# Kernel optimization log

Measured on AMD Instinct MI355X. Metric: run time of the kernel, lower is better.

The kernel has to match this reference:

```python
import jax, jax.numpy as jnp
import numpy as np

EMBED_DIM = 1024
NUM_HEADS = 16
HEAD_DIM = EMBED_DIM // NUM_HEADS


def setup_inputs() -> dict:
    key = jax.random.key(0)
    ks = jax.random.split(key, 9)
    d = EMBED_DIM
    # flax Dense default: lecun_normal kernel init ~ scale 1/sqrt(fan_in), zero bias
    s = 1.0 / np.sqrt(d)
    return {
        "x": jax.random.normal(ks[0], (4, 2048, d), dtype=jnp.float32),
        "Wq": jax.random.normal(ks[1], (d, d), dtype=jnp.float32) * s,
        "bq": jnp.zeros((d,), dtype=jnp.float32),
        "Wk": jax.random.normal(ks[2], (d, d), dtype=jnp.float32) * s,
        "bk": jnp.zeros((d,), dtype=jnp.float32),
        "Wv": jax.random.normal(ks[3], (d, d), dtype=jnp.float32) * s,
        "bv": jnp.zeros((d,), dtype=jnp.float32),
        "Wo": jax.random.normal(ks[4], (d, d), dtype=jnp.float32) * s,
        "bo": jnp.zeros((d,), dtype=jnp.float32),
    }


def reference(x, Wq, bq, Wk, bk, Wv, bv, Wo, bo):
    B, S, D = x.shape
    H, Hd = NUM_HEADS, HEAD_DIM

    def split_heads(t):
        # [B,S,D] -> [B,H,S,Hd]
        return t.reshape(B, S, H, Hd).swapaxes(1, 2)

    q = split_heads(x @ Wq + bq)
    k = split_heads(x @ Wk + bk)
    v = split_heads(x @ Wv + bv)

    # [B,H,S,S] attention logits, scaled by sqrt(head_dim)
    attn_logits = jnp.einsum("bhqd,bhkd->bhqk", q, k) / jnp.sqrt(
        jnp.asarray(Hd, dtype=x.dtype)
    )
    attn = jax.nn.softmax(attn_logits, axis=-1)
    # dropout rate = 0.0 / deterministic=True -> identity

    values = jnp.einsum("bhqk,bhkd->bhqd", attn, v)  # [B,H,S,Hd]
    values = values.swapaxes(1, 2).reshape(B, S, D)  # [B,S,D]
    return values @ Wo + bo
```

## Files before the change

kernel.cpp:

```cpp
#include <hip/hip_runtime.h>
#include <hip/hip_bf16.h>
#include <cstdint>

typedef __attribute__((ext_vector_type(8))) short short8;
typedef __attribute__((ext_vector_type(4))) float f32x4;
typedef __attribute__((ext_vector_type(4))) int int4v;
typedef unsigned short ushort_t;

#define D_MODEL 1024
#define SEQ     2048
#define NBATCH  4
#define NHEADS  16
#define HDIM    64

__device__ __forceinline__ unsigned short f2bf(float f) {
  unsigned int u = __float_as_uint(f);
  u = u + 0x7fffu + ((u >> 16) & 1u);
  return (unsigned short)(u >> 16);
}

__device__ __forceinline__ float exp2_fast(float x) {
  return __builtin_amdgcn_exp2f(x);
}

__device__ __forceinline__ unsigned int cvtpk(float lo, float hi) {
  unsigned int r;
  asm("v_cvt_pk_bf16_f32 %0, %1, %2" : "=v"(r) : "v"(lo), "v"(hi));
  return r;
}

typedef __attribute__((address_space(1))) const void gv_t;
typedef __attribute__((address_space(3))) void lv_t;
__device__ __forceinline__ void gload16(const void* g, void* l) {
  __builtin_amdgcn_global_load_lds((gv_t*)g, (lv_t*)l, 16, 0, 0);
}

__global__ __launch_bounds__(256) void cvt_x_kernel(const float* __restrict__ x,
                                                    ushort_t* __restrict__ xb) {
  int i = blockIdx.x * 256 + threadIdx.x;
  float4 v = reinterpret_cast<const float4*>(x)[i];
  ushort4 o;
  o.x = f2bf(v.x); o.y = f2bf(v.y); o.z = f2bf(v.z); o.w = f2bf(v.w);
  reinterpret_cast<ushort4*>(xb)[i] = o;
}

__global__ __launch_bounds__(256) void cvt_w_kernel(const float* __restrict__ Wq,
                                                    const float* __restrict__ Wk,
                                                    const float* __restrict__ Wv,
                                                    const float* __restrict__ Wo,
                                                    ushort_t* __restrict__ WTqkv,
                                                    ushort_t* __restrict__ WTo) {
  __shared__ float tile[64][65];
  const int z = blockIdx.z;
  const float* W = (z == 0) ? Wq : (z == 1) ? Wk : (z == 2) ? Wv : Wo;
  ushort_t* out = (z < 3) ? (WTqkv + (size_t)z * D_MODEL * D_MODEL) : WTo;
  const int k0 = blockIdx.x * 64, n0 = blockIdx.y * 64;
  const int tx = threadIdx.x & 63, ty = threadIdx.x >> 6;
#pragma unroll
  for (int i = 0; i < 16; ++i) {
    int r = ty + i * 4;
    tile[r][tx] = W[(size_t)(k0 + r) * D_MODEL + n0 + tx];
  }
  __syncthreads();
#pragma unroll
  for (int i = 0; i < 16; ++i) {
    int r = ty + i * 4;
    out[(size_t)(n0 + r) * D_MODEL + k0 + tx] = f2bf(tile[tx][r]);
  }
}

#define BM 128
#define BN 128
#define BK 32
#define QSCALE 0.18033688011112042f

__global__ __launch_bounds__(256) void gemm_qkv_kernel(
    const ushort_t* __restrict__ A, const ushort_t* __restrict__ BT,
    const float* __restrict__ bq, const float* __restrict__ bk,
    const float* __restrict__ bv,
    ushort_t* __restrict__ Qb, ushort_t* __restrict__ Kb,
    ushort_t* __restrict__ Vb) {
  __shared__ __align__(16) ushort_t As[BM * BK];
  __shared__ __align__(16) ushort_t Bs[BN * BK];
  const int t = threadIdx.x;
  const int l = t & 63;
  const int w = t >> 6;
  const int m0 = blockIdx.x * BM;
  const int n0 = blockIdx.y * BN;
  const int wm = (w & 1) * 64, wn = (w >> 1) * 64;
  const int lr = l & 15, lg = l >> 4;

  f32x4 acc[4][4] = {};

  for (int k0 = 0; k0 < D_MODEL; k0 += BK) {
#pragma unroll
    for (int i = 0; i < 2; ++i) {
      int chunk = t + i * 256;
      int row = chunk >> 2;
      int c8 = (chunk & 3) * 8;
      gload16(A  + (size_t)(m0 + row) * D_MODEL + k0 + c8, As + chunk * 8);
      gload16(BT + (size_t)(n0 + row) * D_MODEL + k0 + c8, Bs + chunk * 8);
    }
    __syncthreads();
    short8 af[4], bfr[4];
#pragma unroll
    for (int m = 0; m < 4; ++m)
      af[m] = *reinterpret_cast<const short8*>(As + (wm + m * 16 + lr) * BK + lg * 8);
#pragma unroll
    for (int n = 0; n < 4; ++n)
      bfr[n] = *reinterpret_cast<const short8*>(Bs + (wn + n * 16 + lr) * BK + lg * 8);
#pragma unroll
    for (int m = 0; m < 4; ++m)
#pragma unroll
      for (int n = 0; n < 4; ++n)
        acc[m][n] = __builtin_amdgcn_mfma_f32_16x16x32_bf16(af[m], bfr[n], acc[m][n], 0, 0, 0);
    __syncthreads();
  }

#pragma unroll
  for (int m = 0; m < 4; ++m)
#pragma unroll
    for (int n = 0; n < 4; ++n) {
      int colg = n0 + wn + n * 16 + lr;
      int which = colg >> 10;
      int nc = colg & 1023;
      int h = nc >> 6, hd = nc & 63;
      float bias = (which == 0) ? bq[nc] : (which == 1) ? bk[nc] : bv[nc];
#pragma unroll
      for (int r = 0; r < 4; ++r) {
        int rowg = m0 + wm + m * 16 + lg * 4 + r;
        int b = rowg >> 11, s = rowg & 2047;
        int bh = b * NHEADS + h;
        float vall = acc[m][n][r] + bias;
        if (which == 0) {
          Qb[((size_t)bh * SEQ + s) * HDIM + hd] = f2bf(vall * QSCALE);
        } else if (which == 1) {
          Kb[((size_t)bh * SEQ + s) * HDIM + hd] = f2bf(vall);
        } else {
          Vb[((size_t)bh * HDIM + hd) * SEQ + s] = f2bf(vall);
        }
      }
    }
}

#define KVB 64

__device__ __forceinline__ int kmap(int p) {
  return ((p >> 5) << 5) + (((p >> 2) & 3) << 3) + (((p >> 4) & 1) << 2) + (p & 3);
}

__global__ __launch_bounds__(256) void attn_kernel(const ushort_t* __restrict__ Qb,
                                                   const ushort_t* __restrict__ Kb,
                                                   const ushort_t* __restrict__ Vb,
                                                   ushort_t* __restrict__ Ob) {
  __shared__ __align__(16) ushort_t Kt[2][KVB * HDIM];
  __shared__ __align__(16) ushort_t Vt[2][HDIM * KVB];
  const int t = threadIdx.x, l = t & 63, w = t >> 6;
  const int lr = l & 15, lg = l >> 4;
  const int bh = blockIdx.x;
  const int q0 = blockIdx.y * 64;
  const int b = bh >> 4, h = bh & 15;

  const ushort_t* Qp = Qb + ((size_t)bh * SEQ + q0 + w * 16) * HDIM;
  const ushort_t* Kp = Kb + (size_t)bh * SEQ * HDIM;
  const ushort_t* Vp = Vb + (size_t)bh * HDIM * SEQ;

  const int c0 = t, c1 = t + 256;
  const int r0 = c0 >> 3, col0 = ((c0 & 7) ^ (r0 & 7)) * 8;
  const int r1 = c1 >> 3, col1 = ((c1 & 7) ^ (r1 & 7)) * 8;
  const int kr0 = kmap(r0), kr1 = kmap(r1);

  short8 aq[2];
#pragma unroll
  for (int kk = 0; kk < 2; ++kk)
    aq[kk] = *reinterpret_cast<const short8*>(Qp + lr * HDIM + kk * 32 + lg * 8);

  f32x4 o[4] = {};
  float lsum = 0.f;

  gload16(Kp + (size_t)kr0 * HDIM + col0, &Kt[0][c0 * 8]);
  gload16(Kp + (size_t)kr1 * HDIM + col1, &Kt[0][c1 * 8]);
  gload16(Vp + (size_t)r0 * SEQ + col0, &Vt[0][c0 * 8]);
  gload16(Vp + (size_t)r1 * SEQ + col1, &Vt[0][c1 * 8]);
  __syncthreads();

  int cur = 0;
  for (int kv0 = 0; kv0 < SEQ; kv0 += KVB) {
    if (kv0 + KVB < SEQ) {
      int kvn = kv0 + KVB;
      gload16(Kp + (size_t)(kvn + kr0) * HDIM + col0, &Kt[cur ^ 1][c0 * 8]);
      gload16(Kp + (size_t)(kvn + kr1) * HDIM + col1, &Kt[cur ^ 1][c1 * 8]);
      gload16(Vp + (size_t)r0 * SEQ + kvn + col0, &Vt[cur ^ 1][c0 * 8]);
      gload16(Vp + (size_t)r1 * SEQ + kvn + col1, &Vt[cur ^ 1][c1 * 8]);
    }
    const ushort_t* Kc = Kt[cur];
    const ushort_t* Vc = Vt[cur];
    f32x4 s[4];
#pragma unroll
    for (int n = 0; n < 4; ++n) s[n] = (f32x4){-16.f, -16.f, -16.f, -16.f};
#pragma unroll
    for (int n = 0; n < 4; ++n)
#pragma unroll
      for (int kk = 0; kk < 2; ++kk) {
        short8 ak = *reinterpret_cast<const short8*>(
            Kc + (n * 16 + lr) * HDIM + ((kk * 32 + lg * 8) ^ ((lr & 7) << 3)));
        s[n] = __builtin_amdgcn_mfma_f32_16x16x32_bf16(ak, aq[kk], s[n], 0, 0, 0);
      }
    float ps = 0.f;
#pragma unroll
    for (int n = 0; n < 4; ++n)
#pragma unroll
      for (int r = 0; r < 4; ++r) {
        float p = exp2_fast(s[n][r]);
        s[n][r] = p;
        ps += p;
      }
    ps += __shfl_xor(ps, 16, 64);
    ps += __shfl_xor(ps, 32, 64);
    lsum += ps;
    int4v w0, w1;
    w0[0] = cvtpk(s[0][0], s[0][1]); w0[1] = cvtpk(s[0][2], s[0][3]);
    w0[2] = cvtpk(s[1][0], s[1][1]); w0[3] = cvtpk(s[1][2], s[1][3]);
    w1[0] = cvtpk(s[2][0], s[2][1]); w1[1] = cvtpk(s[2][2], s[2][3]);
    w1[2] = cvtpk(s[3][0], s[3][1]); w1[3] = cvtpk(s[3][2], s[3][3]);
    short8 pb0 = *reinterpret_cast<short8*>(&w0);
    short8 pb1 = *reinterpret_cast<short8*>(&w1);
#pragma unroll
    for (int nd = 0; nd < 4; ++nd) {
      short8 av0 = *reinterpret_cast<const short8*>(
          Vc + (nd * 16 + lr) * KVB + ((lg * 8) ^ ((lr & 7) << 3)));
      o[nd] = __builtin_amdgcn_mfma_f32_16x16x32_bf16(av0, pb0, o[nd], 0, 0, 0);
      short8 av1 = *reinterpret_cast<const short8*>(
          Vc + (nd * 16 + lr) * KVB + ((32 + lg * 8) ^ ((lr & 7) << 3)));
      o[nd] = __builtin_amdgcn_mfma_f32_16x16x32_bf16(av1, pb1, o[nd], 0, 0, 0);
    }
    __syncthreads();
    cur ^= 1;
  }

  float inv = 1.f / lsum;
  size_t orow = ((size_t)b * SEQ + q0 + w * 16 + lr) * D_MODEL + h * HDIM;
#pragma unroll
  for (int nd = 0; nd < 4; ++nd) {
    ushort4 ov;
    ov.x = f2bf(o[nd][0] * inv);
    ov.y = f2bf(o[nd][1] * inv);
    ov.z = f2bf(o[nd][2] * inv);
    ov.w = f2bf(o[nd][3] * inv);
    *reinterpret_cast<ushort4*>(&(((ushort_t*)Ob)[orow + nd * 16 + lg * 4])) = ov;
  }
}

__global__ __launch_bounds__(256) void gemm_out_kernel(const ushort_t* __restrict__ A,
                                                       const ushort_t* __restrict__ BT,
                                                       const float* __restrict__ bo,
                                                       float* __restrict__ out) {
  __shared__ __align__(16) ushort_t As[BM * BK];
  __shared__ __align__(16) ushort_t Bs[BN * BK];
  const int t = threadIdx.x;
  const int l = t & 63;
  const int w = t >> 6;
  const int m0 = blockIdx.x * BM;
  const int n0 = blockIdx.y * BN;
  const int wm = (w & 1) * 64, wn = (w >> 1) * 64;
  const int lr = l & 15, lg = l >> 4;

  f32x4 acc[4][4] = {};

  for (int k0 = 0; k0 < D_MODEL; k0 += BK) {
#pragma unroll
    for (int i = 0; i < 2; ++i) {
      int chunk = t + i * 256;
      int row = chunk >> 2;
      int c8 = (chunk & 3) * 8;
      gload16(A  + (size_t)(m0 + row) * D_MODEL + k0 + c8, As + chunk * 8);
      gload16(BT + (size_t)(n0 + row) * D_MODEL + k0 + c8, Bs + chunk * 8);
    }
    __syncthreads();
    short8 af[4], bfr[4];
#pragma unroll
    for (int m = 0; m < 4; ++m)
      af[m] = *reinterpret_cast<const short8*>(As + (wm + m * 16 + lr) * BK + lg * 8);
#pragma unroll
    for (int n = 0; n < 4; ++n)
      bfr[n] = *reinterpret_cast<const short8*>(Bs + (wn + n * 16 + lr) * BK + lg * 8);
#pragma unroll
    for (int m = 0; m < 4; ++m)
#pragma unroll
      for (int n = 0; n < 4; ++n)
        acc[m][n] = __builtin_amdgcn_mfma_f32_16x16x32_bf16(af[m], bfr[n], acc[m][n], 0, 0, 0);
    __syncthreads();
  }

#pragma unroll
  for (int m = 0; m < 4; ++m)
#pragma unroll
    for (int n = 0; n < 4; ++n) {
      int colg = n0 + wn + n * 16 + lr;
      float bias = bo[colg];
#pragma unroll
      for (int r = 0; r < 4; ++r) {
        int rowg = m0 + wm + m * 16 + lg * 4 + r;
        out[(size_t)rowg * D_MODEL + colg] = acc[m][n][r] + bias;
      }
    }
}

extern "C" void kernel_launch(void* const* d_in, const int* in_sizes, int n_in,
                              void* d_out, int out_size, void* d_ws, size_t ws_size,
                              hipStream_t stream) {
  (void)in_sizes; (void)n_in; (void)out_size; (void)ws_size;
  const float* x  = (const float*)d_in[0];
  const float* Wq = (const float*)d_in[1];
  const float* bq = (const float*)d_in[2];
  const float* Wk = (const float*)d_in[3];
  const float* bk = (const float*)d_in[4];
  const float* Wv = (const float*)d_in[5];
  const float* bv = (const float*)d_in[6];
  const float* Wo = (const float*)d_in[7];
  const float* bo = (const float*)d_in[8];
  float* out = (float*)d_out;

  ushort_t* ws    = (ushort_t*)d_ws;
  ushort_t* WTqkv = ws;
  ushort_t* WTo   = WTqkv + 3145728;
  ushort_t* Qb    = WTo + 1048576;
  ushort_t* Kb    = Qb + 8388608;
  ushort_t* Vb    = Kb + 8388608;
  ushort_t* Ob    = Vb + 8388608;
  ushort_t* xb    = Ob;

  cvt_x_kernel<<<8192, 256, 0, stream>>>(x, xb);
  cvt_w_kernel<<<dim3(16, 16, 4), 256, 0, stream>>>(Wq, Wk, Wv, Wo, WTqkv, WTo);
  gemm_qkv_kernel<<<dim3(64, 24), 256, 0, stream>>>(xb, WTqkv, bq, bk, bv, Qb, Kb, Vb);
  attn_kernel<<<dim3(64, 32), 256, 0, stream>>>(Qb, Kb, Vb, Ob);
  gemm_out_kernel<<<dim3(64, 8), 256, 0, stream>>>(Ob, WTo, bo, out);
}
```

Baseline: 300.1 us.

## Double-buffer GEMM LDS tiles and unroll attention loop with deferred row-sum reduction

The QKV and output projection GEMMs now use two LDS buffers, so the next K tile is prefetched while the current one is consumed, with one barrier per tile instead of two. The attention loop is manually unrolled by two with static buffer indices, which removes the dynamic cur pointer. The per-tile cross-lane shuffle reduction of the softmax row sum moves to after the loop. The goal is to overlap global loads with MFMA work and to cut barrier and shuffle overhead, at the cost of doubled LDS use in the GEMMs, which may lower occupancy.

```diff
diff --git a/kernel.cpp b/kernel.cpp
--- a/kernel.cpp
+++ b/kernel.cpp
@@ -74,14 +74,42 @@
 #define BK 32
 #define QSCALE 0.18033688011112042f
 
+#define GEMM_STAGE(BUF, K0)                                                     \
+  {                                                                             \
+    _Pragma("unroll")                                                           \
+    for (int i = 0; i < 2; ++i) {                                               \
+      int chunk = t + i * 256;                                                  \
+      int row = chunk >> 2;                                                     \
+      int c8 = (chunk & 3) * 8;                                                 \
+      gload16(A  + (size_t)(m0 + row) * D_MODEL + (K0) + c8, As[BUF] + chunk * 8); \
+      gload16(BT + (size_t)(n0 + row) * D_MODEL + (K0) + c8, Bs[BUF] + chunk * 8); \
+    }                                                                           \
+  }
+
+#define GEMM_COMPUTE(BUF)                                                       \
+  {                                                                             \
+    short8 af[4], bfr[4];                                                       \
+    _Pragma("unroll")                                                           \
+    for (int m = 0; m < 4; ++m)                                                 \
+      af[m] = *reinterpret_cast<const short8*>(As[BUF] + (wm + m * 16 + lr) * BK + lg * 8); \
+    _Pragma("unroll")                                                           \
+    for (int n = 0; n < 4; ++n)                                                 \
+      bfr[n] = *reinterpret_cast<const short8*>(Bs[BUF] + (wn + n * 16 + lr) * BK + lg * 8); \
+    _Pragma("unroll")                                                           \
+    for (int m = 0; m < 4; ++m)                                                 \
+      _Pragma("unroll")                                                         \
+      for (int n = 0; n < 4; ++n)                                               \
+        acc[m][n] = __builtin_amdgcn_mfma_f32_16x16x32_bf16(af[m], bfr[n], acc[m][n], 0, 0, 0); \
+  }
+
 __global__ __launch_bounds__(256) void gemm_qkv_kernel(
     const ushort_t* __restrict__ A, const ushort_t* __restrict__ BT,
     const float* __restrict__ bq, const float* __restrict__ bk,
     const float* __restrict__ bv,
     ushort_t* __restrict__ Qb, ushort_t* __restrict__ Kb,
     ushort_t* __restrict__ Vb) {
-  __shared__ __align__(16) ushort_t As[BM * BK];
-  __shared__ __align__(16) ushort_t Bs[BN * BK];
+  __shared__ __align__(16) ushort_t As[2][BM * BK];
+  __shared__ __align__(16) ushort_t Bs[2][BN * BK];
   const int t = threadIdx.x;
   const int l = t & 63;
   const int w = t >> 6;
@@ -92,28 +120,14 @@
 
   f32x4 acc[4][4] = {};
 
-  for (int k0 = 0; k0 < D_MODEL; k0 += BK) {
-#pragma unroll
-    for (int i = 0; i < 2; ++i) {
-      int chunk = t + i * 256;
-      int row = chunk >> 2;
-      int c8 = (chunk & 3) * 8;
-      gload16(A  + (size_t)(m0 + row) * D_MODEL + k0 + c8, As + chunk * 8);
-      gload16(BT + (size_t)(n0 + row) * D_MODEL + k0 + c8, Bs + chunk * 8);
-    }
-    __syncthreads();
-    short8 af[4], bfr[4];
-#pragma unroll
-    for (int m = 0; m < 4; ++m)
-      af[m] = *reinterpret_cast<const short8*>(As + (wm + m * 16 + lr) * BK + lg * 8);
-#pragma unroll
-    for (int n = 0; n < 4; ++n)
-      bfr[n] = *reinterpret_cast<const short8*>(Bs + (wn + n * 16 + lr) * BK + lg * 8);
-#pragma unroll
-    for (int m = 0; m < 4; ++m)
-#pragma unroll
-      for (int n = 0; n < 4; ++n)
-        acc[m][n] = __builtin_amdgcn_mfma_f32_16x16x32_bf16(af[m], bfr[n], acc[m][n], 0, 0, 0);
+  GEMM_STAGE(0, 0);
+  __syncthreads();
+  for (int k0 = 0; k0 < D_MODEL; k0 += 2 * BK) {
+    if (k0 + BK < D_MODEL) GEMM_STAGE(1, k0 + BK);
+    GEMM_COMPUTE(0);
+    __syncthreads();
+    if (k0 + 2 * BK < D_MODEL) GEMM_STAGE(0, k0 + 2 * BK);
+    GEMM_COMPUTE(1);
     __syncthreads();
   }
 
@@ -149,6 +163,53 @@
   return ((p >> 5) << 5) + (((p >> 2) & 3) << 3) + (((p >> 4) & 1) << 2) + (p & 3);
 }
 
+#define ATTN_STAGE(BUF, KVN)                                                    \
+  {                                                                             \
+    gload16(Kp + (size_t)((KVN) + kr0) * HDIM + col0, &Kt[BUF][c0 * 8]);        \
+    gload16(Kp + (size_t)((KVN) + kr1) * HDIM + col1, &Kt[BUF][c1 * 8]);        \
+    gload16(Vp + (size_t)r0 * SEQ + (KVN) + col0, &Vt[BUF][c0 * 8]);            \
+    gload16(Vp + (size_t)r1 * SEQ + (KVN) + col1, &Vt[BUF][c1 * 8]);            \
+  }
+
+#define ATTN_COMPUTE(BUF)                                                       \
+  {                                                                             \
+    f32x4 s[4];                                                                 \
+    _Pragma("unroll")                                                           \
+    for (int n = 0; n < 4; ++n) s[n] = (f32x4){-16.f, -16.f, -16.f, -16.f};     \
+    _Pragma("unroll")                                                           \
+    for (int n = 0; n < 4; ++n)                                                 \
+      _Pragma("unroll")                                                         \
+      for (int kk = 0; kk < 2; ++kk) {                                          \
+        short8 ak = *reinterpret_cast<const short8*>(                           \
+            &Kt[BUF][(n * 16 + lr) * HDIM + ((kk * 32 + lg * 8) ^ ((lr & 7) << 3))]); \
+        s[n] = __builtin_amdgcn_mfma_f32_16x16x32_bf16(ak, aq[kk], s[n], 0, 0, 0); \
+      }                                                                         \
+    _Pragma("unroll")                                                           \
+    for (int n = 0; n < 4; ++n)                                                 \
+      _Pragma("unroll")                                                         \
+      for (int r = 0; r < 4; ++r) {                                             \
+        float p = exp2_fast(s[n][r]);                                           \
+        s[n][r] = p;                                                            \
+        lsum += p;                                                              \
+      }                                                                         \
+    int4v w0, w1;                                                               \
+    w0[0] = cvtpk(s[0][0], s[0][1]); w0[1] = cvtpk(s[0][2], s[0][3]);           \
+    w0[2] = cvtpk(s[1][0], s[1][1]); w0[3] = cvtpk(s[1][2], s[1][3]);           \
+    w1[0] = cvtpk(s[2][0], s[2][1]); w1[1] = cvtpk(s[2][2], s[2][3]);           \
+    w1[2] = cvtpk(s[3][0], s[3][1]); w1[3] = cvtpk(s[3][2], s[3][3]);           \
+    short8 pb0 = *reinterpret_cast<short8*>(&w0);                               \
+    short8 pb1 = *reinterpret_cast<short8*>(&w1);                               \
+    _Pragma("unroll")                                                           \
+    for (int nd = 0; nd < 4; ++nd) {                                            \
+      short8 av0 = *reinterpret_cast<const short8*>(                            \
+          &Vt[BUF][(nd * 16 + lr) * KVB + ((lg * 8) ^ ((lr & 7) << 3))]);       \
+      o[nd] = __builtin_amdgcn_mfma_f32_16x16x32_bf16(av0, pb0, o[nd], 0, 0, 0); \
+      short8 av1 = *reinterpret_cast<const short8*>(                            \
+          &Vt[BUF][(nd * 16 + lr) * KVB + ((32 + lg * 8) ^ ((lr & 7) << 3))]);  \
+      o[nd] = __builtin_amdgcn_mfma_f32_16x16x32_bf16(av1, pb1, o[nd], 0, 0, 0); \
+    }                                                                           \
+  }
+
 __global__ __launch_bounds__(256) void attn_kernel(const ushort_t* __restrict__ Qb,
                                                    const ushort_t* __restrict__ Kb,
                                                    const ushort_t* __restrict__ Vb,
@@ -178,65 +239,20 @@
   f32x4 o[4] = {};
   float lsum = 0.f;
 
-  gload16(Kp + (size_t)kr0 * HDIM + col0, &Kt[0][c0 * 8]);
-  gload16(Kp + (size_t)kr1 * HDIM + col1, &Kt[0][c1 * 8]);
-  gload16(Vp + (size_t)r0 * SEQ + col0, &Vt[0][c0 * 8]);
-  gload16(Vp + (size_t)r1 * SEQ + col1, &Vt[0][c1 * 8]);
+  ATTN_STAGE(0, 0);
   __syncthreads();
 
-  int cur = 0;
-  for (int kv0 = 0; kv0 < SEQ; kv0 += KVB) {
-    if (kv0 + KVB < SEQ) {
-      int kvn = kv0 + KVB;
-      gload16(Kp + (size_t)(kvn + kr0) * HDIM + col0, &Kt[cur ^ 1][c0 * 8]);
-      gload16(Kp + (size_t)(kvn + kr1) * HDIM + col1, &Kt[cur ^ 1][c1 * 8]);
-      gload16(Vp + (size_t)r0 * SEQ + kvn + col0, &Vt[cur ^ 1][c0 * 8]);
-      gload16(Vp + (size_t)r1 * SEQ + kvn + col1, &Vt[cur ^ 1][c1 * 8]);
-    }
-    const ushort_t* Kc = Kt[cur];
-    const ushort_t* Vc = Vt[cur];
-    f32x4 s[4];
-#pragma unroll
-    for (int n = 0; n < 4; ++n) s[n] = (f32x4){-16.f, -16.f, -16.f, -16.f};
-#pragma unroll
-    for (int n = 0; n < 4; ++n)
-#pragma unroll
-      for (int kk = 0; kk < 2; ++kk) {
-        short8 ak = *reinterpret_cast<const short8*>(
-            Kc + (n * 16 + lr) * HDIM + ((kk * 32 + lg * 8) ^ ((lr & 7) << 3)));
-        s[n] = __builtin_amdgcn_mfma_f32_16x16x32_bf16(ak, aq[kk], s[n], 0, 0, 0);
-      }
-    float ps = 0.f;
-#pragma unroll
-    for (int n = 0; n < 4; ++n)
-#pragma unroll
-      for (int r = 0; r < 4; ++r) {
-        float p = exp2_fast(s[n][r]);
-        s[n][r] = p;
-        ps += p;
-      }
-    ps += __shfl_xor(ps, 16, 64);
-    ps += __shfl_xor(ps, 32, 64);
-    lsum += ps;
-    int4v w0, w1;
-    w0[0] = cvtpk(s[0][0], s[0][1]); w0[1] = cvtpk(s[0][2], s[0][3]);
-    w0[2] = cvtpk(s[1][0], s[1][1]); w0[3] = cvtpk(s[1][2], s[1][3]);
-    w1[0] = cvtpk(s[2][0], s[2][1]); w1[1] = cvtpk(s[2][2], s[2][3]);
-    w1[2] = cvtpk(s[3][0], s[3][1]); w1[3] = cvtpk(s[3][2], s[3][3]);
-    short8 pb0 = *reinterpret_cast<short8*>(&w0);
-    short8 pb1 = *reinterpret_cast<short8*>(&w1);
-#pragma unroll
-    for (int nd = 0; nd < 4; ++nd) {
-      short8 av0 = *reinterpret_cast<const short8*>(
-          Vc + (nd * 16 + lr) * KVB + ((lg * 8) ^ ((lr & 7) << 3)));
-      o[nd] = __builtin_amdgcn_mfma_f32_16x16x32_bf16(av0, pb0, o[nd], 0, 0, 0);
-      short8 av1 = *reinterpret_cast<const short8*>(
-          Vc + (nd * 16 + lr) * KVB + ((32 + lg * 8) ^ ((lr & 7) << 3)));
-      o[nd] = __builtin_amdgcn_mfma_f32_16x16x32_bf16(av1, pb1, o[nd], 0, 0, 0);
-    }
-    __syncthreads();
-    cur ^= 1;
-  }
+  for (int kv0 = 0; kv0 < SEQ; kv0 += 2 * KVB) {
+    if (kv0 + KVB < SEQ) ATTN_STAGE(1, kv0 + KVB);
+    ATTN_COMPUTE(0);
+    __syncthreads();
+    if (kv0 + 2 * KVB < SEQ) ATTN_STAGE(0, kv0 + 2 * KVB);
+    ATTN_COMPUTE(1);
+    __syncthreads();
+  }
+
+  lsum += __shfl_xor(lsum, 16, 64);
+  lsum += __shfl_xor(lsum, 32, 64);
 
   float inv = 1.f / lsum;
   size_t orow = ((size_t)b * SEQ + q0 + w * 16 + lr) * D_MODEL + h * HDIM;
@@ -255,8 +271,8 @@
                                                        const ushort_t* __restrict__ BT,
                                                        const float* __restrict__ bo,
                                                        float* __restrict__ out) {
-  __shared__ __align__(16) ushort_t As[BM * BK];
-  __shared__ __align__(16) ushort_t Bs[BN * BK];
+  __shared__ __align__(16) ushort_t As[2][BM * BK];
+  __shared__ __align__(16) ushort_t Bs[2][BN * BK];
   const int t = threadIdx.x;
   const int l = t & 63;
   const int w = t >> 6;
@@ -267,28 +283,14 @@
 
   f32x4 acc[4][4] = {};
 
-  for (int k0 = 0; k0 < D_MODEL; k0 += BK) {
-#pragma unroll
-    for (int i = 0; i < 2; ++i) {
-      int chunk = t + i * 256;
-      int row = chunk >> 2;
-      int c8 = (chunk & 3) * 8;
-      gload16(A  + (size_t)(m0 + row) * D_MODEL + k0 + c8, As + chunk * 8);
-      gload16(BT + (size_t)(n0 + row) * D_MODEL + k0 + c8, Bs + chunk * 8);
-    }
-    __syncthreads();
-    short8 af[4], bfr[4];
-#pragma unroll
-    for (int m = 0; m < 4; ++m)
-      af[m] = *reinterpret_cast<const short8*>(As + (wm + m * 16 + lr) * BK + lg * 8);
-#pragma unroll
-    for (int n = 0; n < 4; ++n)
-      bfr[n] = *reinterpret_cast<const short8*>(Bs + (wn + n * 16 + lr) * BK + lg * 8);
-#pragma unroll
-    for (int m = 0; m < 4; ++m)
-#pragma unroll
-      for (int n = 0; n < 4; ++n)
-        acc[m][n] = __builtin_amdgcn_mfma_f32_16x16x32_bf16(af[m], bfr[n], acc[m][n], 0, 0, 0);
+  GEMM_STAGE(0, 0);
+  __syncthreads();
+  for (int k0 = 0; k0 < D_MODEL; k0 += 2 * BK) {
+    if (k0 + BK < D_MODEL) GEMM_STAGE(1, k0 + BK);
+    GEMM_COMPUTE(0);
+    __syncthreads();
+    if (k0 + 2 * BK < D_MODEL) GEMM_STAGE(0, k0 + 2 * BK);
+    GEMM_COMPUTE(1);
     __syncthreads();
   }
 
```

Result: no change. 295.0 us (-1.7%).
